# Kernel optimization log

Hardware: AMD Instinct MI355X
Metric: run time of the kernel (lower is better)

Reference implementation:

```python
import jax, jax.numpy as jnp
import numpy as np

N, G, F, H, P, OUT = 100000, 64, 64, 128, 2, 2
E = 1_600_000
BN_EPS = 1e-5  # PyG BatchNorm eps; eval mode with running_mean=0, running_var=1


def setup_inputs() -> dict:
    key = jax.random.key(0)
    ks = iter(jax.random.split(key, 64))

    def lin(din, dout):
        w = jax.random.normal(next(ks), (din, dout), jnp.float32) / np.sqrt(din).astype(np.float32)
        return w, jnp.zeros((dout,), jnp.float32)

    inp = {}
    inp["x"] = jax.random.normal(next(ks), (N, F), jnp.float32)
    inp["pos"] = jax.random.normal(next(ks), (N, P), jnp.float32)
    inp["edge_index"] = jax.random.randint(next(ks), (2, E), 0, N, dtype=jnp.int64) if jax.config.jax_enable_x64 else jax.random.randint(next(ks), (2, E), 0, N)
    inp["batch"] = jnp.sort(jax.random.randint(next(ks), (N,), 0, G))
    dims = [F + P, H + P, H + P]
    for l, din in enumerate(dims):
        w1, b1 = lin(din, H)
        w2, b2 = lin(H, H)
        inp[f"w{l}1"], inp[f"b{l}1"] = w1, b1
        inp[f"g{l}1"], inp[f"be{l}1"] = jnp.ones((H,), jnp.float32), jnp.zeros((H,), jnp.float32)
        inp[f"w{l}2"], inp[f"b{l}2"] = w2, b2
        inp[f"g{l}2"], inp[f"be{l}2"] = jnp.ones((H,), jnp.float32), jnp.zeros((H,), jnp.float32)
    inp["wlin"], inp["blin"] = lin(H, OUT)
    return inp


def _bn(h, g, b):
    # eval-mode BatchNorm with running_mean=0, running_var=1
    return h * (g * (1.0 / np.sqrt(1.0 + BN_EPS)).astype(np.float32)) + b


def _mlp(h, w1, b1, g1, be1, w2, b2, g2, be2):
    h = jax.nn.relu(_bn(h @ w1 + b1, g1, be1))
    return jax.nn.relu(_bn(h @ w2 + b2, g2, be2))


def _gin_max(x, src, dst, mlp_params):
    # GINConv with aggr='max', eps=0: mlp(x + max_{j in N(i)} x_j), empty neighborhoods -> 0 (PyG scatter fill)
    agg = jax.ops.segment_max(x[src], dst, num_segments=N)  # [N, C]
    agg = jnp.where(jnp.isneginf(agg), jnp.zeros((), agg.dtype), agg)
    return _mlp(x + agg, *mlp_params)


def reference(x, pos, edge_index, batch,
              w01, b01, g01, be01, w02, b02, g02, be02,
              w11, b11, g11, be11, w12, b12, g12, be12,
              w21, b21, g21, be21, w22, b22, g22, be22,
              wlin, blin):
    src, dst = edge_index[0], edge_index[1]
    h = jnp.concatenate([x, pos], axis=-1)                        # [N, F+P]
    h = _gin_max(h, src, dst, (w01, b01, g01, be01, w02, b02, g02, be02))
    h = jnp.concatenate([h, pos], axis=-1)                        # [N, H+P]
    h = _gin_max(h, src, dst, (w11, b11, g11, be11, w12, b12, g12, be12))
    h = jnp.concatenate([h, pos], axis=-1)
    h = _gin_max(h, src, dst, (w21, b21, g21, be21, w22, b22, g22, be22))
    pooled = jax.ops.segment_max(h, batch, num_segments=G)        # global_max_pool -> [G, H]
    pooled = jnp.where(jnp.isneginf(pooled), jnp.zeros((), pooled.dtype), pooled)
    return pooled @ wlin + blin                                   # logits [G, OUT]
```

## Files before the change

### kernel.cpp

```cpp
#include <hip/hip_runtime.h>
#include <hip/hip_fp16.h>
#include <math.h>
#include <string.h>

constexpr int HDIM = 128;
constexpr int RB   = 136;
constexpr int ZS   = 168;
constexpr float BN_INV = 0.99999500003749980f;

typedef _Float16 half8v __attribute__((ext_vector_type(8)));
typedef __attribute__((ext_vector_type(4))) float float4v;

__device__ __forceinline__ unsigned pkmax(unsigned a, unsigned b) {
  unsigned r;
  asm volatile("v_pk_max_f16 %0, %1, %2" : "=v"(r) : "v"(a), "v"(b));
  return r;
}
__device__ __forceinline__ unsigned pkadd(unsigned a, unsigned b) {
  unsigned r;
  asm volatile("v_pk_add_f16 %0, %1, %2" : "=v"(r) : "v"(a), "v"(b));
  return r;
}

__device__ __forceinline__ float us2f(unsigned short u) { __half h; memcpy(&h, &u, 2); return __half2float(h); }
__device__ __forceinline__ unsigned short f2us(float f) {
  __half h = __float2half(f); unsigned short u; memcpy(&u, &h, 2); return u;
}

__device__ __forceinline__ unsigned encf(float f) {
  unsigned u = __float_as_uint(f);
  return (u & 0x80000000u) ? ~u : (u | 0x80000000u);
}
__device__ __forceinline__ float decf(unsigned u) {
  return (u & 0x80000000u) ? __uint_as_float(u ^ 0x80000000u) : __uint_as_float(~u);
}

__global__ __launch_bounds__(256) void k_bcnt(
    const int* __restrict__ ei, int* __restrict__ bcnt, int E, int shift, int nbkt) {
  __shared__ int hb[256];
  const int tid = threadIdx.x;
  hb[tid] = 0;
  __syncthreads();
  const int base = blockIdx.x * 4096;
#pragma unroll
  for (int k = 0; k < 16; ++k) {
    int e = base + k * 256 + tid;
    if (e < E) atomicAdd(&hb[ei[E + e] >> shift], 1);
  }
  __syncthreads();
  if (tid < nbkt && hb[tid] > 0) atomicAdd(&bcnt[tid], hb[tid]);
}

__global__ __launch_bounds__(256) void k_bscan(
    const int* __restrict__ bcnt, int* __restrict__ bbase, int* __restrict__ gcur,
    int nbkt, int E) {
  __shared__ int s[256];
  int tid = threadIdx.x;
  int v = (tid < nbkt) ? bcnt[tid] : 0;
  s[tid] = v;
  __syncthreads();
  for (int off = 1; off < 256; off <<= 1) {
    int t = (tid >= off) ? s[tid - off] : 0;
    __syncthreads();
    s[tid] += t;
    __syncthreads();
  }
  if (tid < nbkt) {
    int e = s[tid] - v;
    bbase[tid] = e;
    gcur[tid] = e;
  }
  if (tid == 0) bbase[nbkt] = E;
}

__global__ __launch_bounds__(256) void k_bscatter(
    const int* __restrict__ ei, int* __restrict__ gcur,
    unsigned long long* __restrict__ sorted, int E, int shift, int nbkt) {
  __shared__ int hcnt[256];
  __shared__ int hstart[256];
  __shared__ int gbase[256];
  __shared__ unsigned long long sbuf[4096];

  const int tid = threadIdx.x;
  const int base = blockIdx.x * 4096;
  const int validCount = min(4096, E - base);

  hcnt[tid] = 0;
  __syncthreads();

  int sArr[16], dArr[16];
#pragma unroll
  for (int k = 0; k < 16; ++k) {
    int e = base + k * 256 + tid;
    if (e < E) {
      sArr[k] = ei[e];
      dArr[k] = ei[E + e];
      atomicAdd(&hcnt[dArr[k] >> shift], 1);
    } else {
      sArr[k] = -1; dArr[k] = -1;
    }
  }
  __syncthreads();

  {
    int v = hcnt[tid];
    __shared__ int sc[256];
    sc[tid] = v;
    __syncthreads();
    for (int off = 1; off < 256; off <<= 1) {
      int t = (tid >= off) ? sc[tid - off] : 0;
      __syncthreads();
      sc[tid] += t;
      __syncthreads();
    }
    hstart[tid] = sc[tid] - v;
    if (tid < nbkt && v > 0) gbase[tid] = atomicAdd(&gcur[tid], v);
    hcnt[tid] = sc[tid] - v;
  }
  __syncthreads();

#pragma unroll
  for (int k = 0; k < 16; ++k) {
    if (dArr[k] >= 0) {
      int b = dArr[k] >> shift;
      int p = atomicAdd(&hcnt[b], 1);
      sbuf[p] = ((unsigned long long)(unsigned)dArr[k] << 32) | (unsigned)sArr[k];
    }
  }
  __syncthreads();

  for (int p = tid; p < validCount; p += 256) {
    unsigned long long v = sbuf[p];
    int b = (int)(v >> 32) >> shift;
    sorted[(size_t)gbase[b] + (p - hstart[b])] = v;
  }
}

__global__ __launch_bounds__(256) void k_bcsr(
    const unsigned long long* __restrict__ sorted, const int* __restrict__ bbase,
    int* __restrict__ rowptr, int* __restrict__ eidx,
    int shift, int nbkt, int N, int E) {
  __shared__ int cnt[512];
  __shared__ int excl[512];
  __shared__ int sc[256];
  const int b = blockIdx.x, tid = threadIdx.x;
  const int nodeBase = b << shift;
  const int nodesHere = min(512, N - nodeBase);
  const int lo = bbase[b], hi = bbase[b + 1];

  cnt[tid] = 0; cnt[tid + 256] = 0;
  __syncthreads();
  for (int i = lo + tid; i < hi; i += 256) {
    int d = (int)(sorted[i] >> 32);
    atomicAdd(&cnt[d - nodeBase], 1);
  }
  __syncthreads();
  int a0 = cnt[2 * tid], a1 = cnt[2 * tid + 1];
  int pv = a0 + a1;
  sc[tid] = pv;
  __syncthreads();
  for (int off = 1; off < 256; off <<= 1) {
    int t = (tid >= off) ? sc[tid - off] : 0;
    __syncthreads();
    sc[tid] += t;
    __syncthreads();
  }
  int pe = sc[tid] - pv;
  excl[2 * tid] = pe;
  excl[2 * tid + 1] = pe + a0;
  __syncthreads();
  for (int i = tid; i < 512; i += 256) {
    if (i < nodesHere) rowptr[nodeBase + i] = lo + excl[i];
    cnt[i] = excl[i];
  }
  if (b == nbkt - 1 && tid == 0) rowptr[N] = E;
  __syncthreads();
  for (int i = lo + tid; i < hi; i += 256) {
    unsigned long long v = sorted[i];
    int d = (int)(v >> 32);
    int s = (int)(v & 0xFFFFFFFFu);
    int p = atomicAdd(&cnt[d - nodeBase], 1);
    eidx[lo + p] = s;
  }
}

__global__ __launch_bounds__(256) void k_concat0(
    const float* __restrict__ x, const float* __restrict__ pos,
    unsigned short* __restrict__ h0, int N) {
  int r = (int)((blockIdx.x * 256 + threadIdx.x) >> 6);
  if (r >= N) return;
  int lane = threadIdx.x & 63;
  h0[(size_t)r * RB + lane] = f2us(x[(size_t)r * 64 + lane]);
  float pv = (lane < 2) ? pos[(size_t)r * 2 + lane] : 0.0f;
  h0[(size_t)r * RB + 64 + lane] = f2us(pv);
  if (lane < 8) {
    h0[(size_t)r * RB + 128 + lane] = f2us((lane < 2) ? pos[(size_t)r * 2 + lane] : 0.0f);
  }
}

__global__ void k_prepall(const float* __restrict__ w01, const float* __restrict__ w11,
                          const float* __restrict__ w21, const float* __restrict__ w02,
                          const float* __restrict__ w12, const float* __restrict__ w22,
                          unsigned short* __restrict__ Wt) {
  int idx = blockIdx.x * blockDim.x + threadIdx.x;
  if (idx < 61440) {
    int l = idx / 20480, rem = idx % 20480;
    int n = rem / 160, k = rem % 160;
    const float* W = (l == 0) ? w01 : ((l == 1) ? w11 : w21);
    int K = (l == 0) ? 66 : 130;
    float v = (k < K) ? W[(size_t)k * 128 + n] : 0.0f;
    Wt[idx] = f2us(v);
  } else if (idx < 110592) {
    int idx2 = idx - 61440;
    int l = idx2 / 16384, rem = idx2 % 16384;
    int n = rem / 128, k = rem % 128;
    const float* W = (l == 0) ? w02 : ((l == 1) ? w12 : w22);
    Wt[idx] = f2us(W[(size_t)k * 128 + n]);
  }
}

__global__ __launch_bounds__(256) void k_agg(
    const unsigned short* __restrict__ hcat, const int* __restrict__ rowptr,
    const int* __restrict__ eidx, unsigned short* __restrict__ z,
    int actA, int doTail, int N) {
  int wid = (int)((blockIdx.x * 256 + threadIdx.x) >> 6);
  if (wid >= N) return;
  const int lane = threadIdx.x & 63;
  const int half = lane >> 5;
  const int lc = lane & 31;
  const bool act = (lc < actA) || (doTail && lc == 16);
  const int cb = lc * 8;

  const unsigned NEGINF = 0xFC00FC00u;
  unsigned m0 = NEGINF, m1 = NEGINF, m2 = NEGINF, m3 = NEGINF;

  int r0 = rowptr[wid], r1 = rowptr[wid + 1];
  int e = r0 + half;
  for (; e + 2 < r1; e += 4) {
    int sA = eidx[e], sB = eidx[e + 2];
    if (act) {
      uint4 va = *(const uint4*)(hcat + (size_t)sA * RB + cb);
      uint4 vb = *(const uint4*)(hcat + (size_t)sB * RB + cb);
      m0 = pkmax(m0, pkmax(va.x, vb.x));
      m1 = pkmax(m1, pkmax(va.y, vb.y));
      m2 = pkmax(m2, pkmax(va.z, vb.z));
      m3 = pkmax(m3, pkmax(va.w, vb.w));
    }
  }
  for (; e < r1; e += 2) {
    int s = eidx[e];
    if (act) {
      uint4 va = *(const uint4*)(hcat + (size_t)s * RB + cb);
      m0 = pkmax(m0, va.x);
      m1 = pkmax(m1, va.y);
      m2 = pkmax(m2, va.z);
      m3 = pkmax(m3, va.w);
    }
  }

  m0 = pkmax(m0, (unsigned)__shfl_xor((int)m0, 32));
  m1 = pkmax(m1, (unsigned)__shfl_xor((int)m1, 32));
  m2 = pkmax(m2, (unsigned)__shfl_xor((int)m2, 32));
  m3 = pkmax(m3, (unsigned)__shfl_xor((int)m3, 32));

  if (half == 0 && act) {
    if (r0 == r1) { m0 = 0u; m1 = 0u; m2 = 0u; m3 = 0u; }
    uint4 sv = *(const uint4*)(hcat + (size_t)wid * RB + cb);
    uint4 o;
    o.x = pkadd(sv.x, m0);
    o.y = pkadd(sv.y, m1);
    o.z = pkadd(sv.z, m2);
    o.w = pkadd(sv.w, m3);
    *(uint4*)(z + (size_t)wid * RB + cb) = o;
  }
}

__global__ __launch_bounds__(256) void k_mlp(
    const unsigned short* __restrict__ z, int kc1,
    const unsigned short* __restrict__ Wt1,
    const float* __restrict__ b1, const float* __restrict__ g1, const float* __restrict__ e1,
    const unsigned short* __restrict__ Wt2,
    const float* __restrict__ b2, const float* __restrict__ g2, const float* __restrict__ e2,
    unsigned short* __restrict__ out, int N) {
  __shared__ __align__(16) unsigned short zs[4][16][ZS];
  const int tid = threadIdx.x;
  const int w = tid >> 6, lane = tid & 63;
  const int arow = lane & 15;
  const int grp  = lane >> 4;
  const int row0 = blockIdx.x * 64 + w * 16;

  for (int c = lane; c < 16 * 21; c += 64) {
    int r = c / 21, seg = c - r * 21;
    uint4 v = make_uint4(0u, 0u, 0u, 0u);
    if (seg < 17) {
      int gr = row0 + r;
      if (gr >= N) gr = N - 1;
      v = *(const uint4*)(z + (size_t)gr * RB + seg * 8);
    }
    *(uint4*)(&zs[w][r][seg * 8]) = v;
  }

  float4v acc[8];
#pragma unroll
  for (int i = 0; i < 8; ++i) acc[i] = (float4v){0.f, 0.f, 0.f, 0.f};

  for (int kc = 0; kc < kc1; ++kc) {
    half8v a = *(const half8v*)(&zs[w][arow][kc * 32 + grp * 8]);
    const unsigned short* wp = Wt1 + (size_t)arow * 160 + kc * 32 + grp * 8;
#pragma unroll
    for (int nt = 0; nt < 8; ++nt) {
      half8v b = *(const half8v*)(wp + (size_t)(nt * 16) * 160);
      acc[nt] = __builtin_amdgcn_mfma_f32_16x16x32_f16(a, b, acc[nt], 0, 0, 0);
    }
  }

#pragma unroll
  for (int nt = 0; nt < 8; ++nt) {
    int col = nt * 16 + arow;
    float sc = g1[col] * BN_INV;
    float bb = b1[col];
    float be = e1[col];
#pragma unroll
    for (int j = 0; j < 4; ++j) {
      float v = fmaxf(fmaf(acc[nt][j] + bb, sc, be), 0.0f);
      zs[w][grp * 4 + j][col] = f2us(v);
    }
  }

#pragma unroll
  for (int i = 0; i < 8; ++i) acc[i] = (float4v){0.f, 0.f, 0.f, 0.f};
  for (int kc = 0; kc < 4; ++kc) {
    half8v a = *(const half8v*)(&zs[w][arow][kc * 32 + grp * 8]);
    const unsigned short* wp = Wt2 + (size_t)arow * HDIM + kc * 32 + grp * 8;
#pragma unroll
    for (int nt = 0; nt < 8; ++nt) {
      half8v b = *(const half8v*)(wp + (size_t)(nt * 16) * HDIM);
      acc[nt] = __builtin_amdgcn_mfma_f32_16x16x32_f16(a, b, acc[nt], 0, 0, 0);
    }
  }

#pragma unroll
  for (int nt = 0; nt < 8; ++nt) {
    int col = nt * 16 + arow;
    float sc = g2[col] * BN_INV;
    float bb = b2[col];
    float be = e2[col];
#pragma unroll
    for (int j = 0; j < 4; ++j) {
      int gr = row0 + grp * 4 + j;
      if (gr < N) {
        float v = fmaxf(fmaf(acc[nt][j] + bb, sc, be), 0.0f);
        out[(size_t)gr * RB + col] = f2us(v);
      }
    }
  }
}

__global__ void k_pool_init(unsigned* pooled, int GH) {
  int i = blockIdx.x * blockDim.x + threadIdx.x;
  if (i < GH) pooled[i] = 0x007FFFFFu;
}

__global__ __launch_bounds__(128) void k_pool(
    const unsigned short* __restrict__ hcat, const int* __restrict__ batch,
    unsigned* __restrict__ pooled, int N) {
  int base = blockIdx.x * 128;
  int c = threadIdx.x;
  int end = min(base + 128, N);
  int curg = -1;
  float m = -INFINITY;
  for (int i = base; i < end; ++i) {
    int g = batch[i];
    if (g != curg) {
      if (curg >= 0) atomicMax(&pooled[curg * HDIM + c], encf(m));
      curg = g;
      m = -INFINITY;
    }
    m = fmaxf(m, us2f(hcat[(size_t)i * RB + c]));
  }
  if (curg >= 0) atomicMax(&pooled[curg * HDIM + c], encf(m));
}

__global__ __launch_bounds__(64) void k_final(
    const unsigned* __restrict__ pooled, const float* __restrict__ wlin,
    const float* __restrict__ blin, float* __restrict__ out) {
  int g = blockIdx.x;
  int lane = threadIdx.x;
  float v0 = decf(pooled[g * HDIM + lane]);
  float v1 = decf(pooled[g * HDIM + 64 + lane]);
  if (v0 == -INFINITY) v0 = 0.0f;
  if (v1 == -INFINITY) v1 = 0.0f;
  float p0 = v0 * wlin[lane * 2 + 0] + v1 * wlin[(64 + lane) * 2 + 0];
  float p1 = v0 * wlin[lane * 2 + 1] + v1 * wlin[(64 + lane) * 2 + 1];
  for (int off = 32; off > 0; off >>= 1) {
    p0 += __shfl_down(p0, off);
    p1 += __shfl_down(p1, off);
  }
  if (lane == 0) {
    out[g * 2 + 0] = p0 + blin[0];
    out[g * 2 + 1] = p1 + blin[1];
  }
}

static inline size_t ws_align(size_t x) { return (x + 511) & ~(size_t)511; }

extern "C" void kernel_launch(void* const* d_in, const int* in_sizes, int n_in,
                              void* d_out, int out_size, void* d_ws, size_t ws_size,
                              hipStream_t stream) {
  const float* x     = (const float*)d_in[0];
  const float* pos   = (const float*)d_in[1];
  const int*   ei    = (const int*)d_in[2];
  const int*   batch = (const int*)d_in[3];
  const float* wlin  = (const float*)d_in[28];
  const float* blin  = (const float*)d_in[29];

  const int N = in_sizes[3];
  const int E = in_sizes[2] / 2;
  const int G = out_size / 2;

  int shift = 9;
  while ((((N - 1) >> shift) + 1) > 256) ++shift;
  const int nbkt = ((N - 1) >> shift) + 1;

  char* w = (char*)d_ws;
  size_t off = 0;
  auto take = [&](size_t bytes) { void* p = w + off; off += ws_align(bytes); return p; };
  int*            rowptr = (int*)take((size_t)(N + 1) * 4);
  int*            bcnt   = (int*)take(1024);
  int*            bbase  = (int*)take(2048);
  int*            gcur   = (int*)take(1024);
  int*            eidx   = (int*)take((size_t)E * 4);
  unsigned long long* sorted = (unsigned long long*)take((size_t)E * 8);
  unsigned short* hcat   = (unsigned short*)take((size_t)N * RB * 2 + 1024);
  unsigned short* z      = (unsigned short*)take((size_t)N * RB * 2 + 1024);
  unsigned short* Wt     = (unsigned short*)take((size_t)110592 * 2);
  unsigned*       pooled = (unsigned*)take((size_t)G * HDIM * 4);
  (void)ws_size;

  const int chunks = (E + 4095) / 4096;

  hipMemsetAsync(bcnt, 0, 1024, stream);
  k_bcnt<<<chunks, 256, 0, stream>>>(ei, bcnt, E, shift, nbkt);
  k_bscan<<<1, 256, 0, stream>>>(bcnt, bbase, gcur, nbkt, E);
  k_bscatter<<<chunks, 256, 0, stream>>>(ei, gcur, sorted, E, shift, nbkt);
  k_bcsr<<<nbkt, 256, 0, stream>>>(sorted, bbase, rowptr, eidx, shift, nbkt, N, E);

  hipMemsetAsync(z, 0, (size_t)N * RB * 2 + 1024, stream);
  k_concat0<<<(N + 3) / 4, 256, 0, stream>>>(x, pos, hcat, N);
  k_prepall<<<(110592 + 255) / 256, 256, 0, stream>>>(
      (const float*)d_in[4], (const float*)d_in[12], (const float*)d_in[20],
      (const float*)d_in[8], (const float*)d_in[16], (const float*)d_in[24], Wt);

  const int actA[3]   = {9, 16, 16};
  const int doTail[3] = {0, 1, 0};
  const int kc1a[3]   = {3, 5, 5};
  const int aggBlocks = (N + 3) / 4;
  const int mlpBlocks = (N + 63) / 64;

  for (int l = 0; l < 3; ++l) {
    const float* b1 = (const float*)d_in[4 + l * 8 + 1];
    const float* g1 = (const float*)d_in[4 + l * 8 + 2];
    const float* e1 = (const float*)d_in[4 + l * 8 + 3];
    const float* b2 = (const float*)d_in[4 + l * 8 + 5];
    const float* g2 = (const float*)d_in[4 + l * 8 + 6];
    const float* e2 = (const float*)d_in[4 + l * 8 + 7];
    const unsigned short* Wt1 = Wt + (size_t)l * 20480;
    const unsigned short* Wt2 = Wt + 61440 + (size_t)l * 16384;

    k_agg<<<aggBlocks, 256, 0, stream>>>(hcat, rowptr, eidx, z, actA[l], doTail[l], N);
    k_mlp<<<mlpBlocks, 256, 0, stream>>>(z, kc1a[l], Wt1, b1, g1, e1,
                                         Wt2, b2, g2, e2, hcat, N);
  }

  k_pool_init<<<(G * HDIM + 255) / 256, 256, 0, stream>>>(pooled, G * HDIM);
  k_pool<<<(N + 127) / 128, 128, 0, stream>>>(hcat, batch, pooled, N);
  k_final<<<G, 64, 0, stream>>>(pooled, wlin, blin, (float*)d_out);
}
```

Baseline: 541.8 us.

## Fuse prep kernels, precompute BN affine, unroll edge gather, drop memsets

Merges concat, weight transpose, pool init and BN scale/shift precompute into one prep kernel, and removes the z memset and bucket-count memset by writing per-chunk histograms summed in the scan. The MLP epilogue uses precomputed scale and shift. The aggregation loop now gathers four neighbor rows per iteration for more memory-level parallelism. Dropping the z memset leaves padding columns uninitialized, so correctness depends on prior workspace contents.

```diff
diff --git a/kernel.cpp b/kernel.cpp
--- a/kernel.cpp
+++ b/kernel.cpp
@@ -36,7 +36,7 @@
 }
 
 __global__ __launch_bounds__(256) void k_bcnt(
-    const int* __restrict__ ei, int* __restrict__ bcnt, int E, int shift, int nbkt) {
+    const int* __restrict__ ei, int* __restrict__ chunkHist, int E, int shift) {
   __shared__ int hb[256];
   const int tid = threadIdx.x;
   hb[tid] = 0;
@@ -48,15 +48,16 @@
     if (e < E) atomicAdd(&hb[ei[E + e] >> shift], 1);
   }
   __syncthreads();
-  if (tid < nbkt && hb[tid] > 0) atomicAdd(&bcnt[tid], hb[tid]);
+  chunkHist[blockIdx.x * 256 + tid] = hb[tid];
 }
 
 __global__ __launch_bounds__(256) void k_bscan(
-    const int* __restrict__ bcnt, int* __restrict__ bbase, int* __restrict__ gcur,
-    int nbkt, int E) {
+    const int* __restrict__ chunkHist, int chunks,
+    int* __restrict__ bbase, int* __restrict__ gcur, int nbkt, int E) {
   __shared__ int s[256];
   int tid = threadIdx.x;
-  int v = (tid < nbkt) ? bcnt[tid] : 0;
+  int v = 0;
+  for (int c = 0; c < chunks; ++c) v += chunkHist[c * 256 + tid];
   s[tid] = v;
   __syncthreads();
   for (int off = 1; off < 256; off <<= 1) {
@@ -184,38 +185,58 @@
   }
 }
 
-__global__ __launch_bounds__(256) void k_concat0(
-    const float* __restrict__ x, const float* __restrict__ pos,
-    unsigned short* __restrict__ h0, int N) {
-  int r = (int)((blockIdx.x * 256 + threadIdx.x) >> 6);
-  if (r >= N) return;
-  int lane = threadIdx.x & 63;
-  h0[(size_t)r * RB + lane] = f2us(x[(size_t)r * 64 + lane]);
-  float pv = (lane < 2) ? pos[(size_t)r * 2 + lane] : 0.0f;
-  h0[(size_t)r * RB + 64 + lane] = f2us(pv);
-  if (lane < 8) {
-    h0[(size_t)r * RB + 128 + lane] = f2us((lane < 2) ? pos[(size_t)r * 2 + lane] : 0.0f);
-  }
-}
-
-__global__ void k_prepall(const float* __restrict__ w01, const float* __restrict__ w11,
-                          const float* __restrict__ w21, const float* __restrict__ w02,
-                          const float* __restrict__ w12, const float* __restrict__ w22,
-                          unsigned short* __restrict__ Wt) {
-  int idx = blockIdx.x * blockDim.x + threadIdx.x;
-  if (idx < 61440) {
-    int l = idx / 20480, rem = idx % 20480;
+struct PrepArgs {
+  const float *x, *pos;
+  const float *w01, *w11, *w21, *w02, *w12, *w22;
+  const float *b01, *g01, *e01, *b02, *g02, *e02;
+  const float *b11, *g11, *e11, *b12, *g12, *e12;
+  const float *b21, *g21, *e21, *b22, *g22, *e22;
+  unsigned short *h0;
+  unsigned short *Wt;
+  unsigned *pooled;
+  float *Ep;
+  int N, GH;
+};
+
+__global__ __launch_bounds__(256) void k_prep(PrepArgs a) {
+  const int gtid = blockIdx.x * 256 + threadIdx.x;
+
+  if (gtid < a.GH) a.pooled[gtid] = 0x007FFFFFu;
+
+  if (gtid < 61440) {
+    int l = gtid / 20480, rem = gtid % 20480;
     int n = rem / 160, k = rem % 160;
-    const float* W = (l == 0) ? w01 : ((l == 1) ? w11 : w21);
+    const float* W = (l == 0) ? a.w01 : ((l == 1) ? a.w11 : a.w21);
     int K = (l == 0) ? 66 : 130;
     float v = (k < K) ? W[(size_t)k * 128 + n] : 0.0f;
-    Wt[idx] = f2us(v);
-  } else if (idx < 110592) {
-    int idx2 = idx - 61440;
+    a.Wt[gtid] = f2us(v);
+  } else if (gtid < 110592) {
+    int idx2 = gtid - 61440;
     int l = idx2 / 16384, rem = idx2 % 16384;
     int n = rem / 128, k = rem % 128;
-    const float* W = (l == 0) ? w02 : ((l == 1) ? w12 : w22);
-    Wt[idx] = f2us(W[(size_t)k * 128 + n]);
+    const float* W = (l == 0) ? a.w02 : ((l == 1) ? a.w12 : a.w22);
+    a.Wt[gtid] = f2us(W[(size_t)k * 128 + n]);
+  } else if (gtid < 110592 + 768) {
+    int idx = gtid - 110592;
+    int col = idx & 127, stage = (idx >> 7) & 1, l = idx >> 8;
+    const float *bb, *gg, *ee;
+    if (l == 0)      { if (!stage) { bb = a.b01; gg = a.g01; ee = a.e01; } else { bb = a.b02; gg = a.g02; ee = a.e02; } }
+    else if (l == 1) { if (!stage) { bb = a.b11; gg = a.g11; ee = a.e11; } else { bb = a.b12; gg = a.g12; ee = a.e12; } }
+    else             { if (!stage) { bb = a.b21; gg = a.g21; ee = a.e21; } else { bb = a.b22; gg = a.g22; ee = a.e22; } }
+    float s = gg[col] * BN_INV;
+    a.Ep[l * 512 + stage * 256 + col] = s;
+    a.Ep[l * 512 + stage * 256 + 128 + col] = bb[col] * s + ee[col];
+  }
+
+  int r = gtid >> 6;
+  if (r < a.N) {
+    int lane = gtid & 63;
+    a.h0[(size_t)r * RB + lane] = f2us(a.x[(size_t)r * 64 + lane]);
+    float pv = (lane < 2) ? a.pos[(size_t)r * 2 + lane] : 0.0f;
+    a.h0[(size_t)r * RB + 64 + lane] = f2us(pv);
+    if (lane < 8) {
+      a.h0[(size_t)r * RB + 128 + lane] = f2us((lane < 2) ? a.pos[(size_t)r * 2 + lane] : 0.0f);
+    }
   }
 }
 
@@ -236,15 +257,17 @@
 
   int r0 = rowptr[wid], r1 = rowptr[wid + 1];
   int e = r0 + half;
-  for (; e + 2 < r1; e += 4) {
-    int sA = eidx[e], sB = eidx[e + 2];
+  for (; e + 6 < r1; e += 8) {
+    int s0 = eidx[e], s1 = eidx[e + 2], s2 = eidx[e + 4], s3 = eidx[e + 6];
     if (act) {
-      uint4 va = *(const uint4*)(hcat + (size_t)sA * RB + cb);
-      uint4 vb = *(const uint4*)(hcat + (size_t)sB * RB + cb);
-      m0 = pkmax(m0, pkmax(va.x, vb.x));
-      m1 = pkmax(m1, pkmax(va.y, vb.y));
-      m2 = pkmax(m2, pkmax(va.z, vb.z));
-      m3 = pkmax(m3, pkmax(va.w, vb.w));
+      uint4 v0 = *(const uint4*)(hcat + (size_t)s0 * RB + cb);
+      uint4 v1 = *(const uint4*)(hcat + (size_t)s1 * RB + cb);
+      uint4 v2 = *(const uint4*)(hcat + (size_t)s2 * RB + cb);
+      uint4 v3 = *(const uint4*)(hcat + (size_t)s3 * RB + cb);
+      m0 = pkmax(m0, pkmax(pkmax(v0.x, v1.x), pkmax(v2.x, v3.x)));
+      m1 = pkmax(m1, pkmax(pkmax(v0.y, v1.y), pkmax(v2.y, v3.y)));
+      m2 = pkmax(m2, pkmax(pkmax(v0.z, v1.z), pkmax(v2.z, v3.z)));
+      m3 = pkmax(m3, pkmax(pkmax(v0.w, v1.w), pkmax(v2.w, v3.w)));
     }
   }
   for (; e < r1; e += 2) {
@@ -277,10 +300,8 @@
 
 __global__ __launch_bounds__(256) void k_mlp(
     const unsigned short* __restrict__ z, int kc1,
-    const unsigned short* __restrict__ Wt1,
-    const float* __restrict__ b1, const float* __restrict__ g1, const float* __restrict__ e1,
-    const unsigned short* __restrict__ Wt2,
-    const float* __restrict__ b2, const float* __restrict__ g2, const float* __restrict__ e2,
+    const unsigned short* __restrict__ Wt1, const float* __restrict__ Ep1,
+    const unsigned short* __restrict__ Wt2, const float* __restrict__ Ep2,
     unsigned short* __restrict__ out, int N) {
   __shared__ __align__(16) unsigned short zs[4][16][ZS];
   const int tid = threadIdx.x;
@@ -317,12 +338,11 @@
 #pragma unroll
   for (int nt = 0; nt < 8; ++nt) {
     int col = nt * 16 + arow;
-    float sc = g1[col] * BN_INV;
-    float bb = b1[col];
-    float be = e1[col];
+    float sc = Ep1[col];
+    float cc = Ep1[128 + col];
 #pragma unroll
     for (int j = 0; j < 4; ++j) {
-      float v = fmaxf(fmaf(acc[nt][j] + bb, sc, be), 0.0f);
+      float v = fmaxf(fmaf(acc[nt][j], sc, cc), 0.0f);
       zs[w][grp * 4 + j][col] = f2us(v);
     }
   }
@@ -342,23 +362,17 @@
 #pragma unroll
   for (int nt = 0; nt < 8; ++nt) {
     int col = nt * 16 + arow;
-    float sc = g2[col] * BN_INV;
-    float bb = b2[col];
-    float be = e2[col];
+    float sc = Ep2[col];
+    float cc = Ep2[128 + col];
 #pragma unroll
     for (int j = 0; j < 4; ++j) {
       int gr = row0 + grp * 4 + j;
       if (gr < N) {
-        float v = fmaxf(fmaf(acc[nt][j] + bb, sc, be), 0.0f);
+        float v = fmaxf(fmaf(acc[nt][j], sc, cc), 0.0f);
         out[(size_t)gr * RB + col] = f2us(v);
       }
     }
   }
-}
-
-__global__ void k_pool_init(unsigned* pooled, int GH) {
-  int i = blockIdx.x * blockDim.x + threadIdx.x;
-  if (i < GH) pooled[i] = 0x007FFFFFu;
 }
 
 __global__ __launch_bounds__(128) void k_pool(
@@ -421,35 +435,44 @@
   int shift = 9;
   while ((((N - 1) >> shift) + 1) > 256) ++shift;
   const int nbkt = ((N - 1) >> shift) + 1;
+  const int chunks = (E + 4095) / 4096;
 
   char* w = (char*)d_ws;
   size_t off = 0;
   auto take = [&](size_t bytes) { void* p = w + off; off += ws_align(bytes); return p; };
-  int*            rowptr = (int*)take((size_t)(N + 1) * 4);
-  int*            bcnt   = (int*)take(1024);
-  int*            bbase  = (int*)take(2048);
-  int*            gcur   = (int*)take(1024);
-  int*            eidx   = (int*)take((size_t)E * 4);
+  int*            rowptr    = (int*)take((size_t)(N + 1) * 4);
+  int*            chunkHist = (int*)take((size_t)chunks * 256 * 4);
+  int*            bbase     = (int*)take(2048);
+  int*            gcur      = (int*)take(1024);
+  int*            eidx      = (int*)take((size_t)E * 4);
   unsigned long long* sorted = (unsigned long long*)take((size_t)E * 8);
-  unsigned short* hcat   = (unsigned short*)take((size_t)N * RB * 2 + 1024);
-  unsigned short* z      = (unsigned short*)take((size_t)N * RB * 2 + 1024);
-  unsigned short* Wt     = (unsigned short*)take((size_t)110592 * 2);
-  unsigned*       pooled = (unsigned*)take((size_t)G * HDIM * 4);
+  unsigned short* hcat      = (unsigned short*)take((size_t)N * RB * 2 + 1024);
+  unsigned short* z         = (unsigned short*)take((size_t)N * RB * 2 + 1024);
+  unsigned short* Wt        = (unsigned short*)take((size_t)110592 * 2);
+  float*          Ep        = (float*)take(3 * 2 * 2 * 128 * 4);
+  unsigned*       pooled    = (unsigned*)take((size_t)G * HDIM * 4);
   (void)ws_size;
 
-  const int chunks = (E + 4095) / 4096;
-
-  hipMemsetAsync(bcnt, 0, 1024, stream);
-  k_bcnt<<<chunks, 256, 0, stream>>>(ei, bcnt, E, shift, nbkt);
-  k_bscan<<<1, 256, 0, stream>>>(bcnt, bbase, gcur, nbkt, E);
+  k_bcnt<<<chunks, 256, 0, stream>>>(ei, chunkHist, E, shift);
+  k_bscan<<<1, 256, 0, stream>>>(chunkHist, chunks, bbase, gcur, nbkt, E);
   k_bscatter<<<chunks, 256, 0, stream>>>(ei, gcur, sorted, E, shift, nbkt);
   k_bcsr<<<nbkt, 256, 0, stream>>>(sorted, bbase, rowptr, eidx, shift, nbkt, N, E);
 
-  hipMemsetAsync(z, 0, (size_t)N * RB * 2 + 1024, stream);
-  k_concat0<<<(N + 3) / 4, 256, 0, stream>>>(x, pos, hcat, N);
-  k_prepall<<<(110592 + 255) / 256, 256, 0, stream>>>(
-      (const float*)d_in[4], (const float*)d_in[12], (const float*)d_in[20],
-      (const float*)d_in[8], (const float*)d_in[16], (const float*)d_in[24], Wt);
+  {
+    PrepArgs a;
+    a.x = x; a.pos = pos;
+    a.w01 = (const float*)d_in[4];  a.w11 = (const float*)d_in[12]; a.w21 = (const float*)d_in[20];
+    a.w02 = (const float*)d_in[8];  a.w12 = (const float*)d_in[16]; a.w22 = (const float*)d_in[24];
+    a.b01 = (const float*)d_in[5];  a.g01 = (const float*)d_in[6];  a.e01 = (const float*)d_in[7];
+    a.b02 = (const float*)d_in[9];  a.g02 = (const float*)d_in[10]; a.e02 = (const float*)d_in[11];
+    a.b11 = (const float*)d_in[13]; a.g11 = (const float*)d_in[14]; a.e11 = (const float*)d_in[15];
+    a.b12 = (const float*)d_in[17]; a.g12 = (const float*)d_in[18]; a.e12 = (const float*)d_in[19];
+    a.b21 = (const float*)d_in[21]; a.g21 = (const float*)d_in[22]; a.e21 = (const float*)d_in[23];
+    a.b22 = (const float*)d_in[25]; a.g22 = (const float*)d_in[26]; a.e22 = (const float*)d_in[27];
+    a.h0 = hcat; a.Wt = Wt; a.pooled = pooled; a.Ep = Ep;
+    a.N = N; a.GH = G * HDIM;
+    k_prep<<<(N + 3) / 4, 256, 0, stream>>>(a);
+  }
 
   const int actA[3]   = {9, 16, 16};
   const int doTail[3] = {0, 1, 0};
@@ -458,21 +481,15 @@
   const int mlpBlocks = (N + 63) / 64;
 
   for (int l = 0; l < 3; ++l) {
-    const float* b1 = (const float*)d_in[4 + l * 8 + 1];
-    const float* g1 = (const float*)d_in[4 + l * 8 + 2];
-    const float* e1 = (const float*)d_in[4 + l * 8 + 3];
-    const float* b2 = (const float*)d_in[4 + l * 8 + 5];
-    const float* g2 = (const float*)d_in[4 + l * 8 + 6];
-    const float* e2 = (const float*)d_in[4 + l * 8 + 7];
     const unsigned short* Wt1 = Wt + (size_t)l * 20480;
     const unsigned short* Wt2 = Wt + 61440 + (size_t)l * 16384;
+    const float* Ep1 = Ep + l * 512;
+    const float* Ep2 = Ep + l * 512 + 256;
 
     k_agg<<<aggBlocks, 256, 0, stream>>>(hcat, rowptr, eidx, z, actA[l], doTail[l], N);
-    k_mlp<<<mlpBlocks, 256, 0, stream>>>(z, kc1a[l], Wt1, b1, g1, e1,
-                                         Wt2, b2, g2, e2, hcat, N);
-  }
-
-  k_pool_init<<<(G * HDIM + 255) / 256, 256, 0, stream>>>(pooled, G * HDIM);
+    k_mlp<<<mlpBlocks, 256, 0, stream>>>(z, kc1a[l], Wt1, Ep1, Wt2, Ep2, hcat, N);
+  }
+
   k_pool<<<(N + 127) / 128, 128, 0, stream>>>(hcat, batch, pooled, N);
   k_final<<<G, 64, 0, stream>>>(pooled, wlin, blin, (float*)d_out);
 }
```

New measurement: 560.5 us. +3.5%, slower.
